# Performance work log

Measured on AMD Instinct MI355X. Metric: run time of the kernel, lower is better.

The kernel has to match this reference:

```python
import jax, jax.numpy as jnp
import numpy as np

NUM_HEADS = 8
MAX_POINTS = 8


def _sample_one(img, x, y):
    # img: [hd, Hs, Ws]; x, y: [N, P] pixel coords. Bilinear, zeros padding,
    # align_corners=True (caller already converted normalized coords to pixels).
    Hs, Ws = img.shape[-2], img.shape[-1]
    x0f = jnp.floor(x); y0f = jnp.floor(y)
    x0 = x0f.astype(jnp.int32); y0 = y0f.astype(jnp.int32)
    x1 = x0 + 1; y1 = y0 + 1
    wx1 = x - x0f; wx0 = 1.0 - wx1
    wy1 = y - y0f; wy0 = 1.0 - wy1

    def gather(yi, xi):
        valid = ((yi >= 0) & (yi < Hs) & (xi >= 0) & (xi < Ws)).astype(img.dtype)
        yc = jnp.clip(yi, 0, Hs - 1)
        xc = jnp.clip(xi, 0, Ws - 1)
        return img[:, yc, xc] * valid  # [hd, N, P]

    return (gather(y0, x0) * (wy0 * wx0) + gather(y0, x1) * (wy0 * wx1)
            + gather(y1, x0) * (wy1 * wx0) + gather(y1, x1) * (wy1 * wx1))


def _forward(query, ref, q_w, q_b, kv_w, kv_b, off_w, off_b, out_w, out_b, H, W, n_points):
    B, N, C = query.shape
    hd = C // NUM_HEADS
    scale = hd ** -0.5

    q = (query @ q_w + q_b).reshape(B, N, NUM_HEADS, hd)
    # kv_proj is dead code in the source forward (k, v are never used); params kept for parity.

    offsets = (query @ off_w + off_b).reshape(B, N, NUM_HEADS, MAX_POINTS, 2)
    offsets = offsets[:, :, :, :n_points]  # [B, N, nh, P, 2]

    ys = jnp.arange(H, dtype=query.dtype)
    xs = jnp.arange(W, dtype=query.dtype)
    coords = jnp.stack(jnp.meshgrid(ys, xs, indexing='ij'), -1).reshape(N, 2)  # (y, x)
    loc = coords[None, :, None, None, :] + offsets  # [B, N, nh, P, 2]
    g0 = loc[..., 0] / (H - 1) * 2.0 - 1.0
    g1 = loc[..., 1] / (W - 1) * 2.0 - 1.0
    # grid_sample reads grid[...,0] as x and grid[...,1] as y -> faithful to the
    # source's coordinate-channel ordering (channel 0 was normalized with H).
    x_pix = (g0 + 1.0) * 0.5 * (W - 1)
    y_pix = (g1 + 1.0) * 0.5 * (H - 1)

    ref_img = ref.reshape(B, C, H, W)  # faithful to source's .view (raw reinterpret, no permute)
    ref_heads = ref_img.reshape(B, NUM_HEADS, hd, H, W)  # per-head channel slice

    xb = x_pix.transpose(0, 2, 1, 3)  # [B, nh, N, P]
    yb = y_pix.transpose(0, 2, 1, 3)
    sampled = jax.vmap(jax.vmap(_sample_one))(ref_heads, xb, yb)  # [B, nh, hd, N, P]
    sampled = sampled.transpose(0, 3, 1, 4, 2)  # [B, N, nh, P, hd]

    attn = jax.nn.softmax(jnp.einsum('bnhd,bnhpd->bnhp', q, sampled) * scale, axis=-1)
    out = jnp.einsum('bnhp,bnhpd->bnhd', attn, sampled).reshape(B, N, C)
    return out @ out_w + out_b


def setup_inputs():
    key = jax.random.key(0)
    B, H, W, C = 4, 64, 64, 512
    N = H * W
    ks = jax.random.split(key, 8)
    w = lambda k, shp: jax.random.normal(k, shp, jnp.float32) * 0.02
    return {
        'query': jax.random.normal(ks[0], (B, N, C), jnp.float32),
        'ref': jax.random.normal(ks[1], (B, N, C), jnp.float32),
        'q_w': w(ks[2], (C, C)), 'q_b': jnp.zeros((C,), jnp.float32),
        'kv_w': w(ks[3], (C, 2 * C)), 'kv_b': jnp.zeros((2 * C,), jnp.float32),
        'off_w': w(ks[4], (C, NUM_HEADS * MAX_POINTS * 2)),
        'off_b': jnp.zeros((NUM_HEADS * MAX_POINTS * 2,), jnp.float32),
        'out_w': w(ks[5], (C, C)), 'out_b': jnp.zeros((C,), jnp.float32),
        'H': H, 'W': W, 'n_points': 8,
    }


def reference(query, ref, q_w, q_b, kv_w, kv_b, off_w, off_b, out_w, out_b, H, W, n_points):
    return _forward(query, ref, q_w, q_b, kv_w, kv_b, off_w, off_b, out_w, out_b, H, W, n_points)
```

## Files before the change

kernel.cpp:

```cpp
#include <hip/hip_runtime.h>
#include <cmath>

#define NUM_HEADS 8
#define MAX_POINTS 8
#define HD 64
#define SH 64
#define SW 64
#define SC 512

typedef short bf16x8 __attribute__((ext_vector_type(8)));
typedef float f32x4 __attribute__((ext_vector_type(4)));

typedef const __attribute__((address_space(1))) unsigned int gu32;
typedef __attribute__((address_space(3))) unsigned int lu32;

__device__ __forceinline__ unsigned short f2bf(float f) {
    unsigned u = __float_as_uint(f);
    unsigned r = (u + 0x7fff + ((u >> 16) & 1)) >> 16;
    return (unsigned short)r;
}
__device__ __forceinline__ unsigned packbf2(float a, float b) {
    return (unsigned)f2bf(a) | ((unsigned)f2bf(b) << 16);
}
__device__ __forceinline__ void unpack8(uint4 u, float* f) {
    f[0] = __uint_as_float(u.x << 16); f[1] = __uint_as_float(u.x & 0xffff0000u);
    f[2] = __uint_as_float(u.y << 16); f[3] = __uint_as_float(u.y & 0xffff0000u);
    f[4] = __uint_as_float(u.z << 16); f[5] = __uint_as_float(u.z & 0xffff0000u);
    f[6] = __uint_as_float(u.w << 16); f[7] = __uint_as_float(u.w & 0xffff0000u);
}

__global__ __launch_bounds__(256) void cvt_bf16_k(
    const float* __restrict__ in, unsigned short* __restrict__ out, int n)
{
    int i = (blockIdx.x * 256 + threadIdx.x) * 4;
    if (i >= n) return;
    float4 v = *(const float4*)&in[i];
    ushort4 o;
    o.x = f2bf(v.x); o.y = f2bf(v.y); o.z = f2bf(v.z); o.w = f2bf(v.w);
    *(ushort4*)&out[i] = o;
}

__global__ __launch_bounds__(256) void tconv_k(
    const float* __restrict__ in, unsigned short* __restrict__ out, int K, int N)
{
    __shared__ float tile[32][33];
    size_t ib = (size_t)blockIdx.z * K * N;
    int k0 = blockIdx.x * 32, n0 = blockIdx.y * 32;
    int tx = threadIdx.x, ty = threadIdx.y;
#pragma unroll
    for (int i = 0; i < 32; i += 8)
        tile[ty + i][tx] = in[ib + (size_t)(k0 + ty + i) * N + n0 + tx];
    __syncthreads();
#pragma unroll
    for (int i = 0; i < 32; i += 8)
        out[ib + (size_t)(n0 + ty + i) * K + k0 + tx] = f2bf(tile[tx][ty + i]);
}

__device__ __forceinline__ void gemm128_core(
    const unsigned short* A, const unsigned short* BT, int K,
    int bm, int bn, int tid, unsigned short* As, unsigned short* Bs,
    f32x4 (&acc)[4][4])
{
    int wave = tid >> 6, lane = tid & 63;
    int quad = lane >> 4, l16 = lane & 15;
    int wm = (wave >> 1) * 64, wn = (wave & 1) * 64;
    int srow = tid >> 2, sq = (tid & 3) * 8;
    const unsigned short* aP0 = &A[(size_t)(bm + srow) * K + sq];
    const unsigned short* aP1 = aP0 + (size_t)64 * K;
    const unsigned short* bP0 = &BT[(size_t)(bn + srow) * K + sq];
    const unsigned short* bP1 = bP0 + (size_t)64 * K;
    lu32* aL0 = (lu32*)&As[wave * 512];
    lu32* aL1 = (lu32*)&As[2048 + wave * 512];
    lu32* bL0 = (lu32*)&Bs[wave * 512];
    lu32* bL1 = (lu32*)&Bs[2048 + wave * 512];

    for (int k0 = 0; k0 < K; k0 += 32) {
        __builtin_amdgcn_global_load_lds((gu32*)(aP0 + k0), aL0, 16, 0, 0);
        __builtin_amdgcn_global_load_lds((gu32*)(aP1 + k0), aL1, 16, 0, 0);
        __builtin_amdgcn_global_load_lds((gu32*)(bP0 + k0), bL0, 16, 0, 0);
        __builtin_amdgcn_global_load_lds((gu32*)(bP1 + k0), bL1, 16, 0, 0);
        __syncthreads();
        bf16x8 af[4], bfr[4];
#pragma unroll
        for (int t = 0; t < 4; ++t) {
            af[t]  = *(const bf16x8*)&As[(wm + t * 16 + l16) * 32 + quad * 8];
            bfr[t] = *(const bf16x8*)&Bs[(wn + t * 16 + l16) * 32 + quad * 8];
        }
#pragma unroll
        for (int mt = 0; mt < 4; ++mt)
#pragma unroll
            for (int nt = 0; nt < 4; ++nt)
                acc[mt][nt] = __builtin_amdgcn_mfma_f32_16x16x32_bf16(
                    af[mt], bfr[nt], acc[mt][nt], 0, 0, 0);
        __syncthreads();
    }
}

__global__ __launch_bounds__(256) void gemm_qoff_k(
    const unsigned short* __restrict__ A, const unsigned short* __restrict__ BT,
    const float* __restrict__ q_b, const float* __restrict__ off_b,
    unsigned short* __restrict__ qout, float* __restrict__ offout,
    int M, int K)
{
    __shared__ unsigned short As[128 * 32];
    __shared__ unsigned short Bs[128 * 32];
    int tid = threadIdx.x;
    int wave = tid >> 6, lane = tid & 63;
    int quad = lane >> 4, l16 = lane & 15;
    int bm = blockIdx.y * 128, bn = blockIdx.x * 128;
    int wm = (wave >> 1) * 64, wn = (wave & 1) * 64;

    f32x4 acc[4][4];
#pragma unroll
    for (int i = 0; i < 4; ++i)
#pragma unroll
        for (int j = 0; j < 4; ++j) acc[i][j] = (f32x4){0.f, 0.f, 0.f, 0.f};

    gemm128_core(A, BT, K, bm, bn, tid, As, Bs, acc);

#pragma unroll
    for (int mt = 0; mt < 4; ++mt)
#pragma unroll
        for (int nt = 0; nt < 4; ++nt) {
            int r0 = bm + wm + mt * 16 + quad * 4;
            int c  = bn + wn + nt * 16 + l16;
            if (bn < 512) {
                float bv = q_b[c];
#pragma unroll
                for (int r = 0; r < 4; ++r)
                    qout[(size_t)(r0 + r) * 512 + c] = f2bf(acc[mt][nt][r] + bv);
            } else {
                int co = c - 512;
                float bv = off_b[co];
#pragma unroll
                for (int r = 0; r < 4; ++r)
                    offout[(size_t)(r0 + r) * 128 + co] = acc[mt][nt][r] + bv;
            }
        }
}

__global__ __launch_bounds__(256) void gemm_out_k(
    const unsigned short* __restrict__ A, const unsigned short* __restrict__ BT,
    const float* __restrict__ bias, float* __restrict__ Cf, int M, int N, int K)
{
    __shared__ unsigned short As[128 * 32];
    __shared__ unsigned short Bs[128 * 32];
    int tid = threadIdx.x;
    int wave = tid >> 6, lane = tid & 63;
    int quad = lane >> 4, l16 = lane & 15;
    int bm = blockIdx.y * 128, bn = blockIdx.x * 128;
    int wm = (wave >> 1) * 64, wn = (wave & 1) * 64;

    f32x4 acc[4][4];
#pragma unroll
    for (int i = 0; i < 4; ++i)
#pragma unroll
        for (int j = 0; j < 4; ++j) acc[i][j] = (f32x4){0.f, 0.f, 0.f, 0.f};

    gemm128_core(A, BT, K, bm, bn, tid, As, Bs, acc);

#pragma unroll
    for (int mt = 0; mt < 4; ++mt)
#pragma unroll
        for (int nt = 0; nt < 4; ++nt) {
            int r0 = bm + wm + mt * 16 + quad * 4;
            int c  = bn + wn + nt * 16 + l16;
            float bv = bias[c];
#pragma unroll
            for (int r = 0; r < 4; ++r)
                Cf[(size_t)(r0 + r) * N + c] = acc[mt][nt][r] + bv;
        }
}

__global__ __launch_bounds__(256) void sample_attn8_k(
    const unsigned short* __restrict__ qb, const float* __restrict__ offb,
    const unsigned short* __restrict__ refT, unsigned short* __restrict__ ob,
    const int* __restrict__ npp)
{
    int npts = *npp;
    int bn = blockIdx.x * 4 + (threadIdx.x >> 6);
    int lane = threadIdx.x & 63;
    int h = lane >> 3;
    int c8 = (lane & 7) << 3;
    int coff = (h << 6) + c8;
    int b = bn >> 12;
    int n = bn & 4095;
    int row = n >> 6, col = n & 63;

    float qv[8];
    unpack8(*(const uint4*)&qb[(bn << 9) + coff], qv);

    const float* op = offb + (bn << 7) + (h << 4);
    float4 of4[4];
    of4[0] = *(const float4*)(op + 0);
    of4[1] = *(const float4*)(op + 4);
    of4[2] = *(const float4*)(op + 8);
    of4[3] = *(const float4*)(op + 12);
    const float* offs = (const float*)of4;

    const unsigned short* rb = refT + ((size_t)b << 21);

    float sv[MAX_POINTS][8];
    float lg[MAX_POINTS];
#pragma unroll
    for (int p = 0; p < MAX_POINTS; ++p) {
        float x = (float)row + offs[p * 2 + 0];
        float y = (float)col + offs[p * 2 + 1];
        float x0f = floorf(x), y0f = floorf(y);
        int x0 = (int)x0f, y0 = (int)y0f;
        float wx1 = x - x0f, wx0 = 1.f - wx1;
        float wy1 = y - y0f, wy0 = 1.f - wy1;
        float w00 = wy0 * wx0, w01 = wy0 * wx1;
        float w10 = wy1 * wx0, w11 = wy1 * wx1;

        float a8[8];
        if (((unsigned)y0 < 63u) & ((unsigned)x0 < 63u)) {
            const unsigned short* base = rb + (((y0 << 6) + x0) << 9) + coff;
            float s0[8], s1[8], s2[8], s3[8];
            unpack8(*(const uint4*)(base), s0);
            unpack8(*(const uint4*)(base + 512), s1);
            unpack8(*(const uint4*)(base + 32768), s2);
            unpack8(*(const uint4*)(base + 32768 + 512), s3);
#pragma unroll
            for (int j = 0; j < 8; ++j)
                a8[j] = fmaf(w00, s0[j],
                        fmaf(w01, s1[j],
                        fmaf(w10, s2[j], w11 * s3[j])));
        } else {
#pragma unroll
            for (int j = 0; j < 8; ++j) a8[j] = 0.f;
            float wt[4] = {w00, w01, w10, w11};
#pragma unroll
            for (int t = 0; t < 4; ++t) {
                int yi = y0 + (t >> 1);
                int xi = x0 + (t & 1);
                bool ok = ((unsigned)yi < 64u) & ((unsigned)xi < 64u);
                float wv = ok ? wt[t] : 0.f;
                int yc = min(max(yi, 0), 63);
                int xc = min(max(xi, 0), 63);
                float sf[8];
                unpack8(*(const uint4*)&rb[(((yc << 6) + xc) << 9) + coff], sf);
#pragma unroll
                for (int j = 0; j < 8; ++j) a8[j] = fmaf(wv, sf[j], a8[j]);
            }
        }
        float t = 0.f;
#pragma unroll
        for (int j = 0; j < 8; ++j) {
            sv[p][j] = a8[j];
            t = fmaf(qv[j], a8[j], t);
        }
        t += __shfl_xor(t, 1);
        t += __shfl_xor(t, 2);
        t += __shfl_xor(t, 4);
        lg[p] = (p < npts) ? t * 0.125f : -1e30f;
    }

    float mx = -1e30f;
#pragma unroll
    for (int p = 0; p < MAX_POINTS; ++p) mx = fmaxf(mx, lg[p]);
    float ssum = 0.f;
#pragma unroll
    for (int p = 0; p < MAX_POINTS; ++p) {
        lg[p] = __expf(lg[p] - mx);
        ssum += lg[p];
    }
    float inv = 1.f / ssum;

    float o8[8] = {0.f, 0.f, 0.f, 0.f, 0.f, 0.f, 0.f, 0.f};
#pragma unroll
    for (int p = 0; p < MAX_POINTS; ++p)
#pragma unroll
        for (int j = 0; j < 8; ++j) o8[j] = fmaf(lg[p], sv[p][j], o8[j]);

    uint4 o;
    o.x = packbf2(o8[0] * inv, o8[1] * inv);
    o.y = packbf2(o8[2] * inv, o8[3] * inv);
    o.z = packbf2(o8[4] * inv, o8[5] * inv);
    o.w = packbf2(o8[6] * inv, o8[7] * inv);
    *(uint4*)&ob[(bn << 9) + coff] = o;
}

extern "C" void kernel_launch(void* const* d_in, const int* in_sizes, int n_in,
                              void* d_out, int out_size, void* d_ws, size_t ws_size,
                              hipStream_t stream) {
    const float* query = (const float*)d_in[0];
    const float* ref   = (const float*)d_in[1];
    const float* q_w   = (const float*)d_in[2];
    const float* q_b   = (const float*)d_in[3];
    const float* off_w = (const float*)d_in[6];
    const float* off_b = (const float*)d_in[7];
    const float* out_w = (const float*)d_in[8];
    const float* out_b = (const float*)d_in[9];
    const int* npp  = (const int*)d_in[12];

    const int C = 512;
    const int B = 4;
    const int N = 64 * 64;
    const int M = B * N;
    const int OFFD = NUM_HEADS * MAX_POINTS * 2;

    float* offbuf = (float*)d_ws;
    unsigned short* refT_bf = (unsigned short*)(offbuf + (size_t)M * OFFD);
    unsigned short* qin_bf  = refT_bf + (size_t)M * C;
    unsigned short* qbuf_bf = qin_bf  + (size_t)M * C;
    unsigned short* obuf_bf = qbuf_bf + (size_t)M * C;
    unsigned short* wcat    = obuf_bf + (size_t)M * C;
    unsigned short* woutT   = wcat + (size_t)(C + OFFD) * C;

    dim3 blk(256);
    cvt_bf16_k<<<dim3((M * C) / 1024), blk, 0, stream>>>(query, qin_bf, M * C);
    tconv_k<<<dim3(C / 32, C / 32), dim3(32, 8), 0, stream>>>(q_w, wcat, C, C);
    tconv_k<<<dim3(C / 32, OFFD / 32), dim3(32, 8), 0, stream>>>(
        off_w, wcat + (size_t)C * C, C, OFFD);
    tconv_k<<<dim3(C / 32, C / 32), dim3(32, 8), 0, stream>>>(out_w, woutT, C, C);
    tconv_k<<<dim3(C / 32, N / 32, B), dim3(32, 8), 0, stream>>>(ref, refT_bf, C, N);

    gemm_qoff_k<<<dim3(5, M / 128), blk, 0, stream>>>(
        qin_bf, wcat, q_b, off_b, qbuf_bf, offbuf, M, C);

    sample_attn8_k<<<dim3(M / 4), blk, 0, stream>>>(
        qbuf_bf, offbuf, refT_bf, obuf_bf, npp);

    gemm_out_k<<<dim3(C / 128, M / 128), blk, 0, stream>>>(
        obuf_bf, woutT, out_b, (float*)d_out, M, C, C);
}
```

Measured before the change: 220.3 us.

## Merge weight transposes into one launch and shrink sampler register footprint

Three weight transpose-convert launches are merged into a single kernel indexed by blockIdx.z, removing two launch overheads. In the sampling kernel the sampled values are kept packed as bf16 pairs instead of fp32 arrays, offsets are loaded per point as float2, and the interior/border branch is replaced by one unified clamped four-tap path. The aim is fewer live registers and higher occupancy in the gather-bound sampler. In exchange, interior points now pay clamp and mask arithmetic, and rounding the sampled values to bf16 before the weighted sum adds a small precision loss.

```diff
diff --git a/kernel.cpp b/kernel.cpp
--- a/kernel.cpp
+++ b/kernel.cpp
@@ -4,9 +4,6 @@
 #define NUM_HEADS 8
 #define MAX_POINTS 8
 #define HD 64
-#define SH 64
-#define SW 64
-#define SC 512
 
 typedef short bf16x8 __attribute__((ext_vector_type(8)));
 typedef float f32x4 __attribute__((ext_vector_type(4)));
@@ -54,6 +51,29 @@
 #pragma unroll
     for (int i = 0; i < 32; i += 8)
         out[ib + (size_t)(n0 + ty + i) * K + k0 + tx] = f2bf(tile[tx][ty + i]);
+}
+
+__global__ __launch_bounds__(256) void tconvW_k(
+    const float* __restrict__ q_w, const float* __restrict__ off_w,
+    const float* __restrict__ out_w, unsigned short* __restrict__ wcat,
+    unsigned short* __restrict__ woutT)
+{
+    const float* in; unsigned short* out; int N;
+    int z = blockIdx.z;
+    if (z == 0)      { in = q_w;   out = wcat;             N = 512; }
+    else if (z == 1) { in = off_w; out = wcat + 512 * 512; N = 128;
+                       if (blockIdx.y >= 4) return; }
+    else             { in = out_w; out = woutT;            N = 512; }
+    __shared__ float tile[32][33];
+    int k0 = blockIdx.x * 32, n0 = blockIdx.y * 32;
+    int tx = threadIdx.x, ty = threadIdx.y;
+#pragma unroll
+    for (int i = 0; i < 32; i += 8)
+        tile[ty + i][tx] = in[(size_t)(k0 + ty + i) * N + n0 + tx];
+    __syncthreads();
+#pragma unroll
+    for (int i = 0; i < 32; i += 8)
+        out[(size_t)(n0 + ty + i) * 512 + k0 + tx] = f2bf(tile[tx][ty + i]);
 }
 
 __device__ __forceinline__ void gemm128_core(
@@ -191,69 +211,47 @@
     unpack8(*(const uint4*)&qb[(bn << 9) + coff], qv);
 
     const float* op = offb + (bn << 7) + (h << 4);
-    float4 of4[4];
-    of4[0] = *(const float4*)(op + 0);
-    of4[1] = *(const float4*)(op + 4);
-    of4[2] = *(const float4*)(op + 8);
-    of4[3] = *(const float4*)(op + 12);
-    const float* offs = (const float*)of4;
-
-    const unsigned short* rb = refT + ((size_t)b << 21);
-
-    float sv[MAX_POINTS][8];
+    const unsigned short* rb = refT + ((size_t)b << 21) + coff;
+
+    unsigned svp[MAX_POINTS][4];
     float lg[MAX_POINTS];
 #pragma unroll
     for (int p = 0; p < MAX_POINTS; ++p) {
-        float x = (float)row + offs[p * 2 + 0];
-        float y = (float)col + offs[p * 2 + 1];
+        float2 o2 = *(const float2*)(op + p * 2);
+        float x = (float)row + o2.x;
+        float y = (float)col + o2.y;
         float x0f = floorf(x), y0f = floorf(y);
         int x0 = (int)x0f, y0 = (int)y0f;
         float wx1 = x - x0f, wx0 = 1.f - wx1;
         float wy1 = y - y0f, wy0 = 1.f - wy1;
-        float w00 = wy0 * wx0, w01 = wy0 * wx1;
-        float w10 = wy1 * wx0, w11 = wy1 * wx1;
-
-        float a8[8];
-        if (((unsigned)y0 < 63u) & ((unsigned)x0 < 63u)) {
-            const unsigned short* base = rb + (((y0 << 6) + x0) << 9) + coff;
-            float s0[8], s1[8], s2[8], s3[8];
-            unpack8(*(const uint4*)(base), s0);
-            unpack8(*(const uint4*)(base + 512), s1);
-            unpack8(*(const uint4*)(base + 32768), s2);
-            unpack8(*(const uint4*)(base + 32768 + 512), s3);
-#pragma unroll
-            for (int j = 0; j < 8; ++j)
-                a8[j] = fmaf(w00, s0[j],
-                        fmaf(w01, s1[j],
-                        fmaf(w10, s2[j], w11 * s3[j])));
-        } else {
-#pragma unroll
-            for (int j = 0; j < 8; ++j) a8[j] = 0.f;
-            float wt[4] = {w00, w01, w10, w11};
-#pragma unroll
-            for (int t = 0; t < 4; ++t) {
-                int yi = y0 + (t >> 1);
-                int xi = x0 + (t & 1);
-                bool ok = ((unsigned)yi < 64u) & ((unsigned)xi < 64u);
-                float wv = ok ? wt[t] : 0.f;
-                int yc = min(max(yi, 0), 63);
-                int xc = min(max(xi, 0), 63);
-                float sf[8];
-                unpack8(*(const uint4*)&rb[(((yc << 6) + xc) << 9) + coff], sf);
-#pragma unroll
-                for (int j = 0; j < 8; ++j) a8[j] = fmaf(wv, sf[j], a8[j]);
-            }
+        float wt[4] = {wy0 * wx0, wy0 * wx1, wy1 * wx0, wy1 * wx1};
+
+        float a8[8] = {0.f, 0.f, 0.f, 0.f, 0.f, 0.f, 0.f, 0.f};
+#pragma unroll
+        for (int t = 0; t < 4; ++t) {
+            int yi = y0 + (t >> 1);
+            int xi = x0 + (t & 1);
+            bool ok = ((unsigned)yi < 64u) & ((unsigned)xi < 64u);
+            float wv = ok ? wt[t] : 0.f;
+            int yc = min(max(yi, 0), 63);
+            int xc = min(max(xi, 0), 63);
+            float sf[8];
+            unpack8(*(const uint4*)&rb[((yc << 6) + xc) << 9], sf);
+#pragma unroll
+            for (int j = 0; j < 8; ++j) a8[j] = fmaf(wv, sf[j], a8[j]);
         }
         float t = 0.f;
 #pragma unroll
-        for (int j = 0; j < 8; ++j) {
-            sv[p][j] = a8[j];
-            t = fmaf(qv[j], a8[j], t);
-        }
+        for (int j = 0; j < 8; ++j) t = fmaf(qv[j], a8[j], t);
         t += __shfl_xor(t, 1);
         t += __shfl_xor(t, 2);
         t += __shfl_xor(t, 4);
         lg[p] = (p < npts) ? t * 0.125f : -1e30f;
+
+        svp[p][0] = packbf2(a8[0], a8[1]);
+        svp[p][1] = packbf2(a8[2], a8[3]);
+        svp[p][2] = packbf2(a8[4], a8[5]);
+        svp[p][3] = packbf2(a8[6], a8[7]);
     }
 
     float mx = -1e30f;
@@ -269,9 +267,13 @@
 
     float o8[8] = {0.f, 0.f, 0.f, 0.f, 0.f, 0.f, 0.f, 0.f};
 #pragma unroll
-    for (int p = 0; p < MAX_POINTS; ++p)
-#pragma unroll
-        for (int j = 0; j < 8; ++j) o8[j] = fmaf(lg[p], sv[p][j], o8[j]);
+    for (int p = 0; p < MAX_POINTS; ++p) {
+#pragma unroll
+        for (int j = 0; j < 4; ++j) {
+            o8[2 * j + 0] = fmaf(lg[p], __uint_as_float(svp[p][j] << 16), o8[2 * j + 0]);
+            o8[2 * j + 1] = fmaf(lg[p], __uint_as_float(svp[p][j] & 0xffff0000u), o8[2 * j + 1]);
+        }
+    }
 
     uint4 o;
     o.x = packbf2(o8[0] * inv, o8[1] * inv);
@@ -310,10 +312,8 @@
 
     dim3 blk(256);
     cvt_bf16_k<<<dim3((M * C) / 1024), blk, 0, stream>>>(query, qin_bf, M * C);
-    tconv_k<<<dim3(C / 32, C / 32), dim3(32, 8), 0, stream>>>(q_w, wcat, C, C);
-    tconv_k<<<dim3(C / 32, OFFD / 32), dim3(32, 8), 0, stream>>>(
-        off_w, wcat + (size_t)C * C, C, OFFD);
-    tconv_k<<<dim3(C / 32, C / 32), dim3(32, 8), 0, stream>>>(out_w, woutT, C, C);
+    tconvW_k<<<dim3(16, 16, 3), dim3(32, 8), 0, stream>>>(
+        q_w, off_w, out_w, wcat, woutT);
     tconv_k<<<dim3(C / 32, N / 32, B), dim3(32, 8), 0, stream>>>(ref, refT_bf, C, N);
 
     gemm_qoff_k<<<dim3(5, M / 128), blk, 0, stream>>>(
```

Result: no change. 218.3 us (-0.9%).
